# Performance work log

Measured on AMD Instinct MI355X. Metric: run time of the kernel, lower is better.

The kernel has to match this reference:

```python
import jax, jax.numpy as jnp
import numpy as np

N_NODES = 200000
D = 128            # in_channels
B_GRAPHS = 512     # batch_size
STEPS = 3          # processing_steps


def setup_inputs() -> dict:
    key = jax.random.key(0)
    k = jax.random.split(key, 6)
    x = jax.random.normal(k[0], (N_NODES, D), dtype=jnp.float32)
    batch = jnp.sort(jax.random.randint(k[1], (N_NODES,), 0, B_GRAPHS, dtype=jnp.int64))
    s = 0.1
    W_ih = jax.random.normal(k[2], (3 * D, 2 * D), dtype=jnp.float32) * s
    W_hh = jax.random.normal(k[3], (3 * D, D), dtype=jnp.float32) * s
    b_ih = jax.random.normal(k[4], (3 * D,), dtype=jnp.float32) * s
    b_hh = jax.random.normal(k[5], (3 * D,), dtype=jnp.float32) * s
    return {"x": x, "batch": batch, "batch_size": B_GRAPHS,
            "W_ih": W_ih, "W_hh": W_hh, "b_ih": b_ih, "b_hh": b_hh}


def _gru_cell(inp, h, W_ih, W_hh, b_ih, b_hh):
    # inp: [B, 2d], h: [B, d]; PyTorch GRU gate order: r, z, n
    gi = inp @ W_ih.T + b_ih  # [B, 3d]
    gh = h @ W_hh.T + b_hh    # [B, 3d]
    gi_r, gi_z, gi_n = jnp.split(gi, 3, axis=-1)
    gh_r, gh_z, gh_n = jnp.split(gh, 3, axis=-1)
    r = jax.nn.sigmoid(gi_r + gh_r)
    z = jax.nn.sigmoid(gi_z + gh_z)
    n = jnp.tanh(gi_n + r * gh_n)
    return (1.0 - z) * n + z * h


def reference(x, batch, batch_size, W_ih, W_hh, b_ih, b_hh):
    B = batch_size
    d = x.shape[1]
    h = jnp.zeros((B, d), dtype=x.dtype)
    q_star = jnp.zeros((B, 2 * d), dtype=x.dtype)
    for _ in range(STEPS):
        h = _gru_cell(q_star, h, W_ih, W_hh, b_ih, b_hh)
        q = h  # num_layers=1: output == new hidden state
        e = jnp.sum(x * q[batch], axis=-1)  # [N]
        m = jax.ops.segment_max(e, batch, num_segments=B)
        ex = jnp.exp(e - m[batch])
        s = jax.ops.segment_sum(ex, batch, num_segments=B)
        a = ex / (s[batch] + 1e-16)  # segment softmax weights [N]
        r = jax.ops.segment_sum(a[:, None] * x, batch, num_segments=B)  # [B, d]
        q_star = jnp.concatenate([q, r], axis=-1)
    return q_star
```

## Files before the change

kernel.cpp:

```cpp
#include <hip/hip_runtime.h>
#include <math.h>

constexpr int D = 128;
constexpr int B = 512;
constexpr int STEPS = 3;
constexpr int NW_IH = 3 * D * 2 * D;
constexpr int NW_HH = 3 * D * D;

__device__ __forceinline__ float sigmoidf_(float x) { return 1.f / (1.f + __expf(-x)); }
__device__ __forceinline__ float bflo(unsigned int u) { return __uint_as_float(u << 16); }
__device__ __forceinline__ float bfhi(unsigned int u) { return __uint_as_float(u & 0xffff0000u); }
__device__ __forceinline__ unsigned short f2bf_rn(float f) {
    unsigned int u = __float_as_uint(f);
    u += 0x7fffu + ((u >> 16) & 1u);
    return (unsigned short)(u >> 16);
}

__global__ __launch_bounds__(256) void k_prep(const float* __restrict__ Wih,
        const float* __restrict__ Whh, const int* __restrict__ batch, int n,
        unsigned short* __restrict__ wih_bf, unsigned short* __restrict__ whh_bf,
        int* __restrict__ seg) {
    int i = blockIdx.x * blockDim.x + threadIdx.x;
    if (i < NW_IH) wih_bf[i] = f2bf_rn(Wih[i]);
    else if (i < NW_IH + NW_HH) whh_bf[i - NW_IH] = f2bf_rn(Whh[i - NW_IH]);
    if (i <= B) {
        int lo = 0, hi = n;
        while (lo < hi) { int mid = (lo + hi) >> 1; if (batch[mid] < i) lo = mid + 1; else hi = mid; }
        seg[i] = lo;
    }
}

__global__ __launch_bounds__(1024, 8) void k_set2set(
        const float* __restrict__ x,
        const unsigned short* __restrict__ wih_bf,
        const unsigned short* __restrict__ whh_bf,
        const float* __restrict__ bih, const float* __restrict__ bhh,
        const int* __restrict__ seg, float* __restrict__ out) {
    __shared__ float s_q[2 * D];
    __shared__ float s_h[D];
    __shared__ float s_gi[3 * D], s_gh[3 * D];
    __shared__ float sm[32], sl[32];
    __shared__ float s_M, s_inv;
    __shared__ float rpart[16][D];

    const int b = blockIdx.x;
    const int tid = threadIdx.x;
    const int start = seg[b], end = seg[b + 1];
    const int lane32 = tid & 31;
    const int hw = tid >> 5;

    if (tid < 2 * D) s_q[tid] = 0.f;
    if (tid < D) s_h[tid] = 0.f;
    __syncthreads();

    for (int step = 0; step < STEPS; ++step) {
        if (tid < 3 * D) {
            const int t = tid;
            float g0 = bih[t], g1 = 0.f, g2 = 0.f, g3 = 0.f;
            const uint4* wr = (const uint4*)(wih_bf + (size_t)t * (2 * D));
#pragma unroll 4
            for (int c = 0; c < (2 * D) / 8; ++c) {
                uint4 w = wr[c];
                const float* q = &s_q[c * 8];
                g0 = fmaf(bflo(w.x), q[0], g0); g0 = fmaf(bfhi(w.x), q[1], g0);
                g1 = fmaf(bflo(w.y), q[2], g1); g1 = fmaf(bfhi(w.y), q[3], g1);
                g2 = fmaf(bflo(w.z), q[4], g2); g2 = fmaf(bfhi(w.z), q[5], g2);
                g3 = fmaf(bflo(w.w), q[6], g3); g3 = fmaf(bfhi(w.w), q[7], g3);
            }
            s_gi[t] = (g0 + g1) + (g2 + g3);
            float h0 = bhh[t], h1 = 0.f, h2 = 0.f, h3 = 0.f;
            const uint4* vr = (const uint4*)(whh_bf + (size_t)t * D);
#pragma unroll 4
            for (int c = 0; c < D / 8; ++c) {
                uint4 w = vr[c];
                const float* hh = &s_h[c * 8];
                h0 = fmaf(bflo(w.x), hh[0], h0); h0 = fmaf(bfhi(w.x), hh[1], h0);
                h1 = fmaf(bflo(w.y), hh[2], h1); h1 = fmaf(bfhi(w.y), hh[3], h1);
                h2 = fmaf(bflo(w.z), hh[4], h2); h2 = fmaf(bfhi(w.z), hh[5], h2);
                h3 = fmaf(bflo(w.w), hh[6], h3); h3 = fmaf(bfhi(w.w), hh[7], h3);
            }
            s_gh[t] = (h0 + h1) + (h2 + h3);
        }
        __syncthreads();
        if (tid < D) {
            const int t = tid;
            float r  = sigmoidf_(s_gi[t] + s_gh[t]);
            float z  = sigmoidf_(s_gi[D + t] + s_gh[D + t]);
            float nn = tanhf(s_gi[2 * D + t] + r * s_gh[2 * D + t]);
            float hn = (1.f - z) * nn + z * s_h[t];
            s_h[t] = hn;
            s_q[t] = hn;
        }
        __syncthreads();

        const float4 qf = *(const float4*)&s_h[lane32 * 4];
        float m_run = -INFINITY, l_run = 0.f;
        float4 acc = {0.f, 0.f, 0.f, 0.f};
        for (int base = start + hw * 4; base < end; base += 32 * 4) {
            float4 xv0, xv1, xv2, xv3;
            {
                int n0 = base;
                int n1 = (base + 1 < end) ? base + 1 : end - 1;
                int n2 = (base + 2 < end) ? base + 2 : end - 1;
                int n3 = (base + 3 < end) ? base + 3 : end - 1;
                xv0 = ((const float4*)(x + (size_t)n0 * D))[lane32];
                xv1 = ((const float4*)(x + (size_t)n1 * D))[lane32];
                xv2 = ((const float4*)(x + (size_t)n2 * D))[lane32];
                xv3 = ((const float4*)(x + (size_t)n3 * D))[lane32];
            }
            float p0 = fmaf(xv0.x, qf.x, fmaf(xv0.y, qf.y, fmaf(xv0.z, qf.z, xv0.w * qf.w)));
            float p1 = fmaf(xv1.x, qf.x, fmaf(xv1.y, qf.y, fmaf(xv1.z, qf.z, xv1.w * qf.w)));
            float p2 = fmaf(xv2.x, qf.x, fmaf(xv2.y, qf.y, fmaf(xv2.z, qf.z, xv2.w * qf.w)));
            float p3 = fmaf(xv3.x, qf.x, fmaf(xv3.y, qf.y, fmaf(xv3.z, qf.z, xv3.w * qf.w)));
#pragma unroll
            for (int s = 16; s >= 1; s >>= 1) {
                p0 += __shfl_xor(p0, s, 64);
                p1 += __shfl_xor(p1, s, 64);
                p2 += __shfl_xor(p2, s, 64);
                p3 += __shfl_xor(p3, s, 64);
            }
            if (base + 1 >= end) p1 = -INFINITY;
            if (base + 2 >= end) p2 = -INFINITY;
            if (base + 3 >= end) p3 = -INFINITY;

            float cm = fmaxf(fmaxf(p0, p1), fmaxf(p2, p3));
            float nm = fmaxf(m_run, cm);
            float scale = __expf(m_run - nm);
            float a0 = __expf(p0 - nm);
            float a1 = __expf(p1 - nm);
            float a2 = __expf(p2 - nm);
            float a3 = __expf(p3 - nm);
            l_run = fmaf(l_run, scale, (a0 + a1) + (a2 + a3));
            acc.x = fmaf(acc.x, scale, fmaf(a0, xv0.x, fmaf(a1, xv1.x, fmaf(a2, xv2.x, a3 * xv3.x))));
            acc.y = fmaf(acc.y, scale, fmaf(a0, xv0.y, fmaf(a1, xv1.y, fmaf(a2, xv2.y, a3 * xv3.y))));
            acc.z = fmaf(acc.z, scale, fmaf(a0, xv0.z, fmaf(a1, xv1.z, fmaf(a2, xv2.z, a3 * xv3.z))));
            acc.w = fmaf(acc.w, scale, fmaf(a0, xv0.w, fmaf(a1, xv1.w, fmaf(a2, xv2.w, a3 * xv3.w))));
            m_run = nm;
        }
        if (lane32 == 0) { sm[hw] = m_run; sl[hw] = l_run; }
        __syncthreads();
        if (tid == 0) {
            float M = -INFINITY;
            for (int i = 0; i < 32; ++i) M = fmaxf(M, sm[i]);
            float L = 0.f;
            for (int i = 0; i < 32; ++i)
                L += (sm[i] == -INFINITY) ? 0.f : sl[i] * __expf(sm[i] - M);
            s_M = M;
            s_inv = 1.f / (L + 1e-16f);
        }
        __syncthreads();
        const float fac = (m_run == -INFINITY) ? 0.f : __expf(m_run - s_M);
        acc.x *= fac; acc.y *= fac; acc.z *= fac; acc.w *= fac;
        acc.x += __shfl_down(acc.x, 32, 64);
        acc.y += __shfl_down(acc.y, 32, 64);
        acc.z += __shfl_down(acc.z, 32, 64);
        acc.w += __shfl_down(acc.w, 32, 64);
        const int wave = tid >> 6;
        const int lane64 = tid & 63;
        if (lane64 < 32) ((float4*)rpart[wave])[lane64] = acc;
        __syncthreads();
        if (tid < D) {
            float v = 0.f;
#pragma unroll
            for (int w = 0; w < 16; ++w) v += rpart[w][tid];
            s_q[D + tid] = v * s_inv;
        }
        __syncthreads();
    }

    if (tid < 2 * D) out[(size_t)b * (2 * D) + tid] = s_q[tid];
}

extern "C" void kernel_launch(void* const* d_in, const int* in_sizes, int n_in,
                              void* d_out, int out_size, void* d_ws, size_t ws_size,
                              hipStream_t stream) {
    const float* x    = (const float*)d_in[0];
    const int*   batch= (const int*)d_in[1];
    const float* Wih  = (const float*)d_in[3];
    const float* Whh  = (const float*)d_in[4];
    const float* bih  = (const float*)d_in[5];
    const float* bhh  = (const float*)d_in[6];
    const int n = in_sizes[0] / D;

    char* ws = (char*)d_ws;
    int* seg = (int*)ws;
    unsigned short* wih_bf = (unsigned short*)(ws + 4096);
    unsigned short* whh_bf = (unsigned short*)(ws + 4096 + (size_t)NW_IH * 2);

    const int total = NW_IH + NW_HH;
    k_prep<<<(total + 255) / 256, 256, 0, stream>>>(Wih, Whh, batch, n, wih_bf, whh_bf, seg);
    k_set2set<<<B, 1024, 0, stream>>>(x, wih_bf, whh_bf, bih, bhh, seg, (float*)d_out);
}
```

Before: 251.3 us.

## Transpose packed bf16 GRU weights for coalesced loads; shuffle-reduce softmax stats

The prep kernel now stores the bf16 GRU weights as 4-element packs in column-chunk-major order. Adjacent threads (gate rows) therefore read adjacent 8-byte words, which makes the weight matvec loads coalesced instead of each thread striding through its own row. Separately, the serial single-thread merge of 32 partial softmax max/sum pairs is replaced with a wavefront shuffle butterfly. The GRU phase is a small part of the time next to the x streaming, so any gain is likely modest.

```diff
diff --git a/kernel.cpp b/kernel.cpp
--- a/kernel.cpp
+++ b/kernel.cpp
@@ -4,8 +4,9 @@
 constexpr int D = 128;
 constexpr int B = 512;
 constexpr int STEPS = 3;
-constexpr int NW_IH = 3 * D * 2 * D;
-constexpr int NW_HH = 3 * D * D;
+constexpr int ROWS = 3 * D;
+constexpr int NP_IH = (2 * D / 4) * ROWS;
+constexpr int NP_HH = (D / 4) * ROWS;
 
 __device__ __forceinline__ float sigmoidf_(float x) { return 1.f / (1.f + __expf(-x)); }
 __device__ __forceinline__ float bflo(unsigned int u) { return __uint_as_float(u << 16); }
@@ -15,14 +16,25 @@
     u += 0x7fffu + ((u >> 16) & 1u);
     return (unsigned short)(u >> 16);
 }
+__device__ __forceinline__ unsigned int pack2(float a, float b) {
+    return (unsigned int)f2bf_rn(a) | ((unsigned int)f2bf_rn(b) << 16);
+}
 
 __global__ __launch_bounds__(256) void k_prep(const float* __restrict__ Wih,
         const float* __restrict__ Whh, const int* __restrict__ batch, int n,
-        unsigned short* __restrict__ wih_bf, unsigned short* __restrict__ whh_bf,
+        uint2* __restrict__ wih_p, uint2* __restrict__ whh_p,
         int* __restrict__ seg) {
     int i = blockIdx.x * blockDim.x + threadIdx.x;
-    if (i < NW_IH) wih_bf[i] = f2bf_rn(Wih[i]);
-    else if (i < NW_IH + NW_HH) whh_bf[i - NW_IH] = f2bf_rn(Whh[i - NW_IH]);
+    if (i < NP_IH) {
+        int c = i / ROWS, t = i - c * ROWS;
+        const float* src = Wih + (size_t)t * (2 * D) + 4 * c;
+        wih_p[i] = make_uint2(pack2(src[0], src[1]), pack2(src[2], src[3]));
+    } else if (i < NP_IH + NP_HH) {
+        int j = i - NP_IH;
+        int c = j / ROWS, t = j - c * ROWS;
+        const float* src = Whh + (size_t)t * D + 4 * c;
+        whh_p[j] = make_uint2(pack2(src[0], src[1]), pack2(src[2], src[3]));
+    }
     if (i <= B) {
         int lo = 0, hi = n;
         while (lo < hi) { int mid = (lo + hi) >> 1; if (batch[mid] < i) lo = mid + 1; else hi = mid; }
@@ -32,8 +44,8 @@
 
 __global__ __launch_bounds__(1024, 8) void k_set2set(
         const float* __restrict__ x,
-        const unsigned short* __restrict__ wih_bf,
-        const unsigned short* __restrict__ whh_bf,
+        const uint2* __restrict__ wih_p,
+        const uint2* __restrict__ whh_p,
         const float* __restrict__ bih, const float* __restrict__ bhh,
         const int* __restrict__ seg, float* __restrict__ out) {
     __shared__ float s_q[2 * D];
@@ -54,32 +66,32 @@
     __syncthreads();
 
     for (int step = 0; step < STEPS; ++step) {
-        if (tid < 3 * D) {
+        if (tid < ROWS) {
             const int t = tid;
-            float g0 = bih[t], g1 = 0.f, g2 = 0.f, g3 = 0.f;
-            const uint4* wr = (const uint4*)(wih_bf + (size_t)t * (2 * D));
-#pragma unroll 4
-            for (int c = 0; c < (2 * D) / 8; ++c) {
-                uint4 w = wr[c];
-                const float* q = &s_q[c * 8];
-                g0 = fmaf(bflo(w.x), q[0], g0); g0 = fmaf(bfhi(w.x), q[1], g0);
-                g1 = fmaf(bflo(w.y), q[2], g1); g1 = fmaf(bfhi(w.y), q[3], g1);
-                g2 = fmaf(bflo(w.z), q[4], g2); g2 = fmaf(bfhi(w.z), q[5], g2);
-                g3 = fmaf(bflo(w.w), q[6], g3); g3 = fmaf(bfhi(w.w), q[7], g3);
-            }
-            s_gi[t] = (g0 + g1) + (g2 + g3);
-            float h0 = bhh[t], h1 = 0.f, h2 = 0.f, h3 = 0.f;
-            const uint4* vr = (const uint4*)(whh_bf + (size_t)t * D);
-#pragma unroll 4
-            for (int c = 0; c < D / 8; ++c) {
-                uint4 w = vr[c];
-                const float* hh = &s_h[c * 8];
-                h0 = fmaf(bflo(w.x), hh[0], h0); h0 = fmaf(bfhi(w.x), hh[1], h0);
-                h1 = fmaf(bflo(w.y), hh[2], h1); h1 = fmaf(bfhi(w.y), hh[3], h1);
-                h2 = fmaf(bflo(w.z), hh[4], h2); h2 = fmaf(bfhi(w.z), hh[5], h2);
-                h3 = fmaf(bflo(w.w), hh[6], h3); h3 = fmaf(bfhi(w.w), hh[7], h3);
-            }
-            s_gh[t] = (h0 + h1) + (h2 + h3);
+            float a0 = bih[t], a1 = 0.f, a2 = 0.f, a3 = 0.f;
+            const uint2* P = wih_p + t;
+#pragma unroll 8
+            for (int c = 0; c < (2 * D) / 4; ++c) {
+                uint2 w = P[(size_t)c * ROWS];
+                const float* q = &s_q[c * 4];
+                a0 = fmaf(bflo(w.x), q[0], a0);
+                a1 = fmaf(bfhi(w.x), q[1], a1);
+                a2 = fmaf(bflo(w.y), q[2], a2);
+                a3 = fmaf(bfhi(w.y), q[3], a3);
+            }
+            s_gi[t] = (a0 + a1) + (a2 + a3);
+            float b0 = bhh[t], b1 = 0.f, b2 = 0.f, b3 = 0.f;
+            const uint2* Q = whh_p + t;
+#pragma unroll 8
+            for (int c = 0; c < D / 4; ++c) {
+                uint2 w = Q[(size_t)c * ROWS];
+                const float* hh = &s_h[c * 4];
+                b0 = fmaf(bflo(w.x), hh[0], b0);
+                b1 = fmaf(bfhi(w.x), hh[1], b1);
+                b2 = fmaf(bflo(w.y), hh[2], b2);
+                b3 = fmaf(bfhi(w.y), hh[3], b3);
+            }
+            s_gh[t] = (b0 + b1) + (b2 + b3);
         }
         __syncthreads();
         if (tid < D) {
@@ -139,14 +151,18 @@
         }
         if (lane32 == 0) { sm[hw] = m_run; sl[hw] = l_run; }
         __syncthreads();
-        if (tid == 0) {
-            float M = -INFINITY;
-            for (int i = 0; i < 32; ++i) M = fmaxf(M, sm[i]);
-            float L = 0.f;
-            for (int i = 0; i < 32; ++i)
-                L += (sm[i] == -INFINITY) ? 0.f : sl[i] * __expf(sm[i] - M);
-            s_M = M;
-            s_inv = 1.f / (L + 1e-16f);
+        if (tid < 64) {
+            float m = sm[tid & 31], l = sl[tid & 31];
+#pragma unroll
+            for (int s = 16; s >= 1; s >>= 1) {
+                float mo = __shfl_xor(m, s, 64);
+                float lo = __shfl_xor(l, s, 64);
+                float nm2 = fmaxf(m, mo);
+                float t1 = (m  == -INFINITY) ? 0.f : l  * __expf(m  - nm2);
+                float t2 = (mo == -INFINITY) ? 0.f : lo * __expf(mo - nm2);
+                l = t1 + t2; m = nm2;
+            }
+            if (tid == 0) { s_M = m; s_inv = 1.f / (l + 1e-16f); }
         }
         __syncthreads();
         const float fac = (m_run == -INFINITY) ? 0.f : __expf(m_run - s_M);
@@ -184,10 +200,10 @@
 
     char* ws = (char*)d_ws;
     int* seg = (int*)ws;
-    unsigned short* wih_bf = (unsigned short*)(ws + 4096);
-    unsigned short* whh_bf = (unsigned short*)(ws + 4096 + (size_t)NW_IH * 2);
-
-    const int total = NW_IH + NW_HH;
-    k_prep<<<(total + 255) / 256, 256, 0, stream>>>(Wih, Whh, batch, n, wih_bf, whh_bf, seg);
-    k_set2set<<<B, 1024, 0, stream>>>(x, wih_bf, whh_bf, bih, bhh, seg, (float*)d_out);
-}
+    uint2* wih_p = (uint2*)(ws + 4096);
+    uint2* whh_p = (uint2*)(ws + 4096 + (size_t)NP_IH * sizeof(uint2));
+
+    const int total = NP_IH + NP_HH;
+    k_prep<<<(total + 255) / 256, 256, 0, stream>>>(Wih, Whh, batch, n, wih_p, whh_p, seg);
+    k_set2set<<<B, 1024, 0, stream>>>(x, wih_p, whh_p, bih, bhh, seg, (float*)d_out);
+}
```

Result: slower. 264.6 us (+5.3%).
